# Kernel optimization log

Hardware: AMD Instinct MI355X
Metric: run time of the kernel (lower is better)

## Reference

```python
import jax
import jax.numpy as jnp
import numpy as np

N = 16384        # total input points (single batch: o = [N])
C_IN = 64        # in_planes
C_OUT = 128      # out_planes
NSAMPLE = 16     # neighbors per sampled point
STRIDE = 4       # -> new_stride = 2, FPS samples N//2 points
BN_EPS = 1e-5


def setup_inputs() -> dict:
    key = jax.random.key(0)
    k1, k2, k3 = jax.random.split(key, 3)
    p = jax.random.normal(k1, (N, 3), dtype=jnp.float32)
    x = jax.random.normal(k2, (N, C_IN), dtype=jnp.float32)
    o = jnp.array([N], dtype=jnp.int32)  # single-batch offset
    W = jax.random.normal(k3, (3 + C_IN, C_OUT), dtype=jnp.float32) * 0.05
    gamma = jnp.ones((C_OUT,), dtype=jnp.float32)
    beta = jnp.zeros((C_OUT,), dtype=jnp.float32)
    return {"p": p, "x": x, "o": o, "W": W, "gamma": gamma, "beta": beta}


def fps(p, m):
    """Furthest point sampling: returns m indices into p [N,3], starting at 0."""
    n = p.shape[0]
    def step(carry, _):
        dists, last = carry  # dists: [N] min sq-dist to selected set
        d = jnp.sum((p - p[last]) ** 2, axis=-1)
        dists = jnp.minimum(dists, d)
        nxt = jnp.argmax(dists).astype(jnp.int32)
        return (dists, nxt), nxt
    init = (jnp.full((n,), 1e10, dtype=p.dtype), jnp.int32(0))
    _, rest = jax.lax.scan(step, init, None, length=m - 1)
    return jnp.concatenate([jnp.zeros((1,), jnp.int32), rest])


def knn_idx(q, p, k):
    """Indices of k nearest points in p [N,3] for each query in q [m,3]."""
    d = (jnp.sum(q * q, -1, keepdims=True)
         - 2.0 * (q @ p.T)
         + jnp.sum(p * p, -1))  # [m, N]
    _, idx = jax.lax.top_k(-d, k)
    return idx


def group_mlp_pool(q, p, x, W, gamma, beta):
    """queryandgroup(use_xyz=True) -> linear -> BN(train) -> ReLU -> maxpool(nsample)."""
    idx = knn_idx(q, p, NSAMPLE)                      # [m, k]
    rel = p[idx] - q[:, None, :]                       # [m, k, 3] relative xyz
    feats = jnp.concatenate([rel, x[idx]], axis=-1)    # [m, k, 3+C_IN]
    h = feats @ W                                      # [m, k, C_OUT]
    # BatchNorm1d in training mode: stats over (m, k) per channel
    mean = jnp.mean(h, axis=(0, 1))
    var = jnp.var(h, axis=(0, 1))
    h = (h - mean) * jax.lax.rsqrt(var + BN_EPS) * gamma + beta
    h = jax.nn.relu(h)
    return jnp.max(h, axis=1)                          # [m, C_OUT]


def reference(p, x, o, W, gamma, beta):
    m_total = N // (STRIDE // 2)       # 8192 sampled points
    idx = fps(p, m_total)
    m1 = m_total // 2 + m_total % 2    # first half (ceil)
    idx1, idx2 = idx[:m1], idx[m1:]
    n_p, n_p2 = p[idx1], p[idx2]
    x1 = group_mlp_pool(n_p, p, x, W, gamma, beta)
    x2 = group_mlp_pool(n_p2, p, x, W, gamma, beta)
    n_o = jnp.array([m1], dtype=jnp.int32)
    n_o2 = jnp.array([m_total - m1], dtype=jnp.int32)
    return (n_p, x1, n_o, n_p2, x2, n_o2)
```

## Files before the change

kernel.cpp:

```cpp
#include <hip/hip_runtime.h>

#define N_PTS 16384
#define M_TOTAL 8192
#define M1 4096

#define OUT_NP   0
#define OUT_X1   12288
#define OUT_NO   536576
#define OUT_NP2  536577
#define OUT_X2   548865
#define OUT_NO2  1073153

#define POOL_C 64

__global__ void k0_init(const float* __restrict__ p, float* __restrict__ sump,
                        float* __restrict__ px, float* __restrict__ py, float* __restrict__ pz,
                        float* __restrict__ out, int* __restrict__ flag, int* __restrict__ fidx,
                        double* __restrict__ bn) {
    int i = blockIdx.x * 256 + threadIdx.x;
    if (i == 0) { out[OUT_NO] = 4096.0f; out[OUT_NO2] = 4096.0f; atomicExch(flag, 0); }
    if (i < 512) bn[i] = 0.0;
    if (i < M_TOTAL) fidx[i] = (i == 0) ? 0 : -1;
    if (i < N_PTS) {
        float x = p[3*i], y = p[3*i+1], z = p[3*i+2];
        px[i] = x; py[i] = y; pz[i] = z;
        sump[i] = __fadd_rn(__fadd_rn(__fmul_rn(x,x), __fmul_rn(y,y)), __fmul_rn(z,z));
    }
}

__device__ __forceinline__ unsigned spread4(unsigned v) {
    return (v & 1u) | ((v & 2u) << 2) | ((v & 4u) << 4) | ((v & 8u) << 6);
}
__device__ __forceinline__ float bb_d2(float qx, float qy, float qz,
                                       float mnx, float mxx, float mny, float mxy,
                                       float mnz, float mxz) {
    float ax = fmaxf(fmaxf(__fsub_rn(mnx, qx), __fsub_rn(qx, mxx)), 0.0f);
    float ay = fmaxf(fmaxf(__fsub_rn(mny, qy), __fsub_rn(qy, mxy)), 0.0f);
    float az = fmaxf(fmaxf(__fsub_rn(mnz, qz), __fsub_rn(qz, mxz)), 0.0f);
    return __fadd_rn(__fadd_rn(__fmul_rn(ax,ax), __fmul_rn(ay,ay)), __fmul_rn(az,az));
}
__device__ __forceinline__ float pt_d2(float ax, float ay, float az,
                                       float bx, float by, float bz) {
    float dx = __fsub_rn(ax,bx), dy = __fsub_rn(ay,by), dz = __fsub_rn(az,bz);
    return __fadd_rn(__fadd_rn(__fmul_rn(dx,dx), __fmul_rn(dy,dy)), __fmul_rn(dz,dz));
}
__device__ __forceinline__ float wave_max64(float v) {
    v = fmaxf(v, __int_as_float(__builtin_amdgcn_update_dpp(0, __float_as_int(v), 0x111, 0xf, 0xf, true)));
    v = fmaxf(v, __int_as_float(__builtin_amdgcn_update_dpp(0, __float_as_int(v), 0x112, 0xf, 0xf, true)));
    v = fmaxf(v, __int_as_float(__builtin_amdgcn_update_dpp(0, __float_as_int(v), 0x114, 0xf, 0xf, true)));
    v = fmaxf(v, __int_as_float(__builtin_amdgcn_update_dpp(0, __float_as_int(v), 0x118, 0xf, 0xf, true)));
    v = fmaxf(v, __int_as_float(__builtin_amdgcn_update_dpp(0, __float_as_int(v), 0x142, 0xf, 0xf, true)));
    v = fmaxf(v, __int_as_float(__builtin_amdgcn_update_dpp(0, __float_as_int(v), 0x143, 0xf, 0xf, true)));
    return __int_as_float(__builtin_amdgcn_readlane(__float_as_int(v), 63));
}

__global__ __launch_bounds__(1024) void k1_fps(
    const float* __restrict__ p,
    float* __restrict__ rx, float* __restrict__ ry, float* __restrict__ rz,
    int* __restrict__ rid,
    int* __restrict__ fidx, float* __restrict__ out, int* __restrict__ flag,
    const float* __restrict__ px, const float* __restrict__ py,
    const float* __restrict__ pz, const float* __restrict__ sump,
    const float* __restrict__ xin, const float* __restrict__ W,
    float* __restrict__ hmax, float* __restrict__ hmin,
    double* __restrict__ bn)
{
    int tid = threadIdx.x, lane = tid & 63, wv = tid >> 6;

    __shared__ int hist[4096];
    __shared__ float sred[16][6];
    __shared__ int wsum[16];
    __shared__ float4 pool4[POOL_C];
    __shared__ unsigned ppk[POOL_C];
    __shared__ float4 barr4[POOL_C+1];
    __shared__ unsigned skeys[POOL_C];
    __shared__ float fdv[16];
    __shared__ unsigned fdk[16];
    __shared__ unsigned mcell;
    __shared__ float s_invm;
    __shared__ int s_cutbin;
    __shared__ unsigned s_cutbits;
    __shared__ unsigned s_fkey;
    __shared__ int bcnt, tcell;
    __shared__ float sdk[4][16][64];
    __shared__ int   sik[4][16][64];

    if (blockIdx.x != 0) {
        float a0 = 1.0f + tid, a1 = 2.0f, a2 = 3.0f, a3 = 4.0f;
        const float hb = 1.0000001f, hc = 1e-9f;
        if (wv < 4) {
            int g = (blockIdx.x - 1) * 4 + wv;
            for (int jq = 0; jq < 9; ++jq) {
                int q = g + 1020 * jq;
                if (q >= M_TOTAL) break;
                int qi = -1;
                for (;;) {
                    if (lane == 0)
                        qi = __hip_atomic_load(&fidx[q], __ATOMIC_RELAXED, __HIP_MEMORY_SCOPE_AGENT);
                    qi = __shfl(qi, 0);
                    if (qi >= 0) break;
#pragma unroll
                    for (int u = 0; u < 256; ++u) {
                        a0 = __fmaf_rn(a0, hb, hc); a1 = __fmaf_rn(a1, hb, hc);
                        a2 = __fmaf_rn(a2, hb, hc); a3 = __fmaf_rn(a3, hb, hc);
                    }
                }
                float qx = px[qi], qy = py[qi], qz = pz[qi], sq = sump[qi];
                float bd[16]; int bi[16];
#pragma unroll
                for (int k = 0; k < 16; ++k) { bd[k] = 3.4e38f; bi[k] = 0x7fffffff; }
                for (int j0 = 0; j0 < N_PTS; j0 += 64) {
                    int j = j0 + lane;
                    float dot = __fmaf_rn(pz[j], qz, __fmaf_rn(py[j], qy, __fmul_rn(px[j], qx)));
                    float d = __fadd_rn(__fsub_rn(sq, __fmul_rn(2.0f, dot)), sump[j]);
                    if (d < bd[15]) {
                        float cdv = d; int ci = j;
#pragma unroll
                        for (int k = 0; k < 16; ++k) {
                            if (cdv < bd[k]) { float td = bd[k]; int ti = bi[k]; bd[k] = cdv; bi[k] = ci; cdv = td; ci = ti; }
                        }
                    }
                }
#pragma unroll
                for (int k = 0; k < 16; ++k) { sdk[wv][k][lane] = bd[k]; sik[wv][k][lane] = bi[k]; }
                int njr[16];
                int pos = 0;
#pragma unroll
                for (int r = 0; r < 16; ++r) {
                    float hd = (pos < 16) ? sdk[wv][pos][lane] : 3.4e38f;
                    int   hi2 = (pos < 16) ? sik[wv][pos][lane] : 0x7fffffff;
                    float md = hd; int mi = hi2;
#pragma unroll
                    for (int off = 1; off < 64; off <<= 1) {
                        float od = __shfl_xor(md, off);
                        int   oi = __shfl_xor(mi, off);
                        if (od < md || (od == md && oi < mi)) { md = od; mi = oi; }
                    }
                    if (hi2 == mi && pos < 16) pos++;
                    njr[r] = mi;
                }

                float hmx0 = -3.4e38f, hmn0 = 3.4e38f, hmx1 = -3.4e38f, hmn1 = 3.4e38f;
                double sm0 = 0.0, sq0 = 0.0, sm1 = 0.0, sq1 = 0.0;
#pragma unroll
                for (int s2 = 0; s2 < 16; ++s2) {
                    int nj = njr[s2];
                    float acc0 = 0.0f, acc1 = 0.0f;
                    {
                        float f0 = p[3*nj+0] - qx;
                        acc0 = __fmaf_rn(f0, W[0*128 + lane], acc0);
                        acc1 = __fmaf_rn(f0, W[0*128 + 64 + lane], acc1);
                        float f1 = p[3*nj+1] - qy;
                        acc0 = __fmaf_rn(f1, W[1*128 + lane], acc0);
                        acc1 = __fmaf_rn(f1, W[1*128 + 64 + lane], acc1);
                        float f2 = p[3*nj+2] - qz;
                        acc0 = __fmaf_rn(f2, W[2*128 + lane], acc0);
                        acc1 = __fmaf_rn(f2, W[2*128 + 64 + lane], acc1);
                    }
                    const float* xr = &xin[nj*64];
                    for (int j = 3; j < 67; ++j) {
                        float f = xr[j-3];
                        acc0 = __fmaf_rn(f, W[j*128 + lane], acc0);
                        acc1 = __fmaf_rn(f, W[j*128 + 64 + lane], acc1);
                    }
                    hmx0 = fmaxf(hmx0, acc0); hmn0 = fminf(hmn0, acc0);
                    hmx1 = fmaxf(hmx1, acc1); hmn1 = fminf(hmn1, acc1);
                    sm0 += (double)acc0; sq0 += (double)acc0 * (double)acc0;
                    sm1 += (double)acc1; sq1 += (double)acc1 * (double)acc1;
                }
                hmax[q*128 + lane]      = hmx0;  hmax[q*128 + 64 + lane] = hmx1;
                hmin[q*128 + lane]      = hmn0;  hmin[q*128 + 64 + lane] = hmn1;
                int hb2 = (q >= M1) ? 128 : 0;
                atomicAdd(&bn[hb2 + lane],            sm0);
                atomicAdd(&bn[hb2 + 64 + lane],       sm1);
                atomicAdd(&bn[256 + hb2 + lane],      sq0);
                atomicAdd(&bn[256 + hb2 + 64 + lane], sq1);
            }
        }
        for (;;) {
#pragma unroll
            for (int u = 0; u < 512; ++u) {
                a0 = __fmaf_rn(a0, hb, hc); a1 = __fmaf_rn(a1, hb, hc);
                a2 = __fmaf_rn(a2, hb, hc); a3 = __fmaf_rn(a3, hb, hc);
            }
            int done = 0;
            if (lane == 0)
                done = __hip_atomic_load(flag, __ATOMIC_RELAXED, __HIP_MEMORY_SCOPE_AGENT);
            done = __shfl(done, 0);
            if (done) break;
        }
        __asm__ volatile("" :: "v"(a0), "v"(a1), "v"(a2), "v"(a3));
        return;
    }

    float mnx = 3.4e38f, mny = 3.4e38f, mnz = 3.4e38f;
    float mxx = -3.4e38f, mxy = -3.4e38f, mxz = -3.4e38f;
#pragma unroll
    for (int k = 0; k < 16; ++k) {
        int i = tid + 1024*k;
        float x = p[3*i], y = p[3*i+1], z = p[3*i+2];
        mnx = fminf(mnx, x); mxx = fmaxf(mxx, x);
        mny = fminf(mny, y); mxy = fmaxf(mxy, y);
        mnz = fminf(mnz, z); mxz = fmaxf(mxz, z);
    }
#pragma unroll
    for (int off = 1; off < 64; off <<= 1) {
        mnx = fminf(mnx, __shfl_xor(mnx, off)); mxx = fmaxf(mxx, __shfl_xor(mxx, off));
        mny = fminf(mny, __shfl_xor(mny, off)); mxy = fmaxf(mxy, __shfl_xor(mxy, off));
        mnz = fminf(mnz, __shfl_xor(mnz, off)); mxz = fmaxf(mxz, __shfl_xor(mxz, off));
    }
    if (lane == 0) {
        sred[wv][0] = mnx; sred[wv][1] = mxx; sred[wv][2] = mny;
        sred[wv][3] = mxy; sred[wv][4] = mnz; sred[wv][5] = mxz;
    }
    for (int j = tid; j < 4096; j += 1024) hist[j] = 0;
    __syncthreads();
    mnx = sred[0][0]; mxx = sred[0][1]; mny = sred[0][2];
    mxy = sred[0][3]; mnz = sred[0][4]; mxz = sred[0][5];
    for (int w2 = 1; w2 < 16; ++w2) {
        mnx = fminf(mnx, sred[w2][0]); mxx = fmaxf(mxx, sred[w2][1]);
        mny = fminf(mny, sred[w2][2]); mxy = fmaxf(mxy, sred[w2][3]);
        mnz = fminf(mnz, sred[w2][4]); mxz = fmaxf(mxz, sred[w2][5]);
    }
    float sx = 16.0f / fmaxf(mxx - mnx, 1e-20f);
    float sy = 16.0f / fmaxf(mxy - mny, 1e-20f);
    float sz = 16.0f / fmaxf(mxz - mnz, 1e-20f);

    int mcode[16];
#pragma unroll
    for (int k = 0; k < 16; ++k) {
        int i = tid + 1024*k;
        float x = p[3*i], y = p[3*i+1], z = p[3*i+2];
        int cx = min(15, (int)((x - mnx) * sx));
        int cy = min(15, (int)((y - mny) * sy));
        int cz = min(15, (int)((z - mnz) * sz));
        int m = (int)(spread4((unsigned)cx) | (spread4((unsigned)cy) << 1) | (spread4((unsigned)cz) << 2));
        mcode[k] = m;
        atomicAdd(&hist[m], 1);
    }
    __syncthreads();
    {
        int c0 = hist[4*tid], c1 = hist[4*tid+1], c2 = hist[4*tid+2], c3 = hist[4*tid+3];
        int lsum = c0 + c1 + c2 + c3;
        int incl = lsum;
#pragma unroll
        for (int off = 1; off < 64; off <<= 1) {
            int n = __shfl_up(incl, off);
            if (lane >= off) incl += n;
        }
        if (lane == 63) wsum[wv] = incl;
        __syncthreads();
        int woff = 0;
        for (int j = 0; j < wv; ++j) woff += wsum[j];
        int excl = woff + incl - lsum;
        hist[4*tid]   = excl;
        hist[4*tid+1] = excl + c0;
        hist[4*tid+2] = excl + c0 + c1;
        hist[4*tid+3] = excl + c0 + c1 + c2;
    }
    __syncthreads();
#pragma unroll
    for (int k = 0; k < 16; ++k) {
        int i = tid + 1024*k;
        int pos = atomicAdd(&hist[mcode[k]], 1);
        rx[pos] = p[3*i]; ry[pos] = p[3*i+1]; rz[pos] = p[3*i+2];
        rid[pos] = i;
    }
    __syncthreads();

    int base = tid * 16;
    float ld[16];
    float bmnx = 3.4e38f, bmny = 3.4e38f, bmnz = 3.4e38f;
    float bmxx = -3.4e38f, bmxy = -3.4e38f, bmxz = -3.4e38f;
#pragma unroll
    for (int k = 0; k < 16; ++k) {
        float x = rx[base+k], y = ry[base+k], z = rz[base+k];
        ld[k] = 1e10f;
        bmnx = fminf(bmnx, x); bmxx = fmaxf(bmxx, x);
        bmny = fminf(bmny, y); bmxy = fmaxf(bmxy, y);
        bmnz = fminf(bmnz, z); bmxz = fmaxf(bmxz, z);
    }
    float wsmnx = bmnx, wsmxx = bmxx, wsmny = bmny, wsmxy = bmxy, wsmnz = bmnz, wsmxz = bmxz;
#pragma unroll
    for (int off = 1; off < 64; off <<= 1) {
        wsmnx = fminf(wsmnx, __shfl_xor(wsmnx, off)); wsmxx = fmaxf(wsmxx, __shfl_xor(wsmxx, off));
        wsmny = fminf(wsmny, __shfl_xor(wsmny, off)); wsmxy = fmaxf(wsmxy, __shfl_xor(wsmxy, off));
        wsmnz = fminf(wsmnz, __shfl_xor(wsmnz, off)); wsmxz = fmaxf(wsmxz, __shfl_xor(wsmxz, off));
    }
    float gmax = 1e10f, wave_gmax = 1e10f;

    if (tid == 0) {
        float x0 = p[0], y0 = p[1], z0 = p[2];
        out[OUT_NP+0] = x0; out[OUT_NP+1] = y0; out[OUT_NP+2] = z0;
        barr4[0] = make_float4(x0, y0, z0, 0.0f);
        skeys[0] = 0u;
        bcnt = 1; tcell = 1; mcell = 0u;
    }

    for (;;) {
        __syncthreads();
        int t_now = tcell;
        int s = bcnt;
        if (tid < s)
            __hip_atomic_store(&fidx[t_now - s + tid], (int)skeys[tid], __ATOMIC_RELAXED, __HIP_MEMORY_SCOPE_AGENT);
        if (t_now >= M_TOTAL) break;

        {
            bool dirtyw = false;
            if (lane < s) {
                float4 cc = barr4[lane];
                dirtyw = bb_d2(cc.x, cc.y, cc.z, wsmnx, wsmxx, wsmny, wsmxy, wsmnz, wsmxz) < wave_gmax;
            }
            unsigned long long mm = __ballot(dirtyw);
            if (mm) {
                float gx[16], gy[16], gz[16];
#pragma unroll
                for (int k = 0; k < 16; ++k) { gx[k] = rx[base+k]; gy[k] = ry[base+k]; gz[k] = rz[base+k]; }
                while (mm) {
                    int b = __builtin_ctzll(mm); mm &= mm - 1;
                    float4 cc = barr4[b];
                    if (bb_d2(cc.x, cc.y, cc.z, bmnx, bmxx, bmny, bmxy, bmnz, bmxz) < gmax) {
#pragma unroll
                        for (int k = 0; k < 16; ++k)
                            ld[k] = fminf(ld[k], pt_d2(gx[k], gy[k], gz[k], cc.x, cc.y, cc.z));
                    }
                }
            }
        }
        gmax = ld[0];
#pragma unroll
        for (int k = 1; k < 16; ++k) gmax = fmaxf(gmax, ld[k]);
        wave_gmax = wave_max64(gmax);
        if (lane == 0) atomicMax(&mcell, __float_as_uint(wave_gmax));
        if (tid < 130) hist[tid] = 0;
        __syncthreads();
        if (tid == 0) { s_invm = 1.0f / __uint_as_float(mcell); mcell = 0u; }
        __syncthreads();
        float invm = s_invm;
#pragma unroll
        for (int k = 0; k < 16; ++k) {
            unsigned u = __float_as_uint(__fmul_rn(ld[k], invm));
            if (u >= 0x3F000000u) {
                int bin = 16256 - (int)(u >> 16);
                bin = bin < 0 ? 0 : (bin > 128 ? 128 : bin);
                atomicAdd(&hist[bin], 1);
            }
        }
        __syncthreads();
        if (wv == 0) {
            int b0 = hist[2*lane], b1 = hist[2*lane+1];
            int pair = b0 + b1;
            int incl = pair;
#pragma unroll
            for (int off = 1; off < 64; off <<= 1) { int n = __shfl_up(incl, off); if (lane >= off) incl += n; }
            int before = incl - pair;
            int cb = 0;
            if (before + b0 <= POOL_C) cb = 2*lane + 1;
            if (before + pair <= POOL_C) cb = 2*lane + 2;
            if (lane == 63) { if (incl + hist[128] <= POOL_C) cb = 129; }
#pragma unroll
            for (int off = 1; off < 64; off <<= 1) cb = max(cb, __shfl_xor(cb, off));
            if (lane == 0) { s_cutbin = cb; s_cutbits = (unsigned)(16257 - cb) << 16; }
        }
        __syncthreads();

        unsigned cutbits = s_cutbits;
        int cl = 0;
#pragma unroll
        for (int k = 0; k < 16; ++k)
            cl += (__float_as_uint(__fmul_rn(ld[k], invm)) >= cutbits) ? 1 : 0;
        int inc3 = cl;
#pragma unroll
        for (int off = 1; off < 64; off <<= 1) { int n = __shfl_up(inc3, off); if (lane >= off) inc3 += n; }
        if (lane == 63) wsum[wv] = inc3;
        __syncthreads();
        int woff2 = 0, ptot = 0;
        for (int j = 0; j < 16; ++j) { int wsj = wsum[j]; if (j < wv) woff2 += wsj; ptot += wsj; }

        if (s_cutbin == 0 || ptot == 0) {
            float bv = -1.0f; unsigned bk = 0xffffffffu;
#pragma unroll
            for (int k = 0; k < 16; ++k) {
                unsigned kk = ((unsigned)rid[base+k] << 14) | (unsigned)(base + k);
                bool better = (ld[k] > bv) || (ld[k] == bv && kk < bk);
                bv = better ? ld[k] : bv; bk = better ? kk : bk;
            }
#pragma unroll
            for (int off = 1; off < 64; off <<= 1) {
                float ov = __shfl_xor(bv, off); unsigned ok = __shfl_xor(bk, off);
                bool better = (ov > bv) || (ov == bv && ok < bk);
                bv = better ? ov : bv; bk = better ? ok : bk;
            }
            if (lane == 0) { fdv[wv] = bv; fdk[wv] = bk; }
            __syncthreads();
            if (tid < 64) {
                float v2 = (tid < 16) ? fdv[tid] : -1.0f;
                unsigned k2v = (tid < 16) ? fdk[tid] : 0xffffffffu;
#pragma unroll
                for (int off = 1; off < 16; off <<= 1) {
                    float ov = __shfl_xor(v2, off); unsigned ok = __shfl_xor(k2v, off);
                    bool better = (ov > v2) || (ov == v2 && ok < k2v);
                    v2 = better ? ov : v2; k2v = better ? ok : k2v;
                }
                if (tid == 0) {
                    s_fkey = k2v;
                    int pos = (int)(k2v & 16383u);
                    __hip_atomic_store(&fidx[t_now], (int)(k2v >> 14), __ATOMIC_RELAXED, __HIP_MEMORY_SCOPE_AGENT);
                    float wx = rx[pos], wy = ry[pos], wz = rz[pos];
                    int o = (t_now < M1) ? (OUT_NP + 3*t_now) : (OUT_NP2 + 3*(t_now - M1));
                    out[o] = wx; out[o+1] = wy; out[o+2] = wz;
                    tcell = t_now + 1; bcnt = 0;
                }
            }
            __syncthreads();
            {
                int pos = (int)(s_fkey & 16383u);
                float wx = rx[pos], wy = ry[pos], wz = rz[pos];
                if (bb_d2(wx, wy, wz, bmnx, bmxx, bmny, bmxy, bmnz, bmxz) < gmax) {
#pragma unroll
                    for (int k = 0; k < 16; ++k)
                        ld[k] = fminf(ld[k], pt_d2(rx[base+k], ry[base+k], rz[base+k], wx, wy, wz));
                }
            }
            continue;
        }

        int nb = woff2 + inc3 - cl;
#pragma unroll
        for (int k = 0; k < 16; ++k) {
            if (__float_as_uint(__fmul_rn(ld[k], invm)) >= cutbits) {
                pool4[nb] = make_float4(rx[base+k], ry[base+k], rz[base+k], ld[k]);
                ppk[nb] = (unsigned)rid[base+k];
                nb++;
            }
        }
        if (tid >= ptot && tid < POOL_C) {
            pool4[tid] = make_float4(0.0f, 0.0f, 0.0f, 0.0f);
            ppk[tid] = 0x7fffffffu;
        }
        __syncthreads();

        if (wv == 0) {
            __builtin_amdgcn_s_setprio(3);
            float4 e = pool4[lane];
            float ex = e.x, ey = e.y, ez = e.z, dv = e.w;
            unsigned key = ppk[lane];
            int tl = t_now, bc = 0;
            float mw = wave_max64(dv);
            while (__float_as_uint(__fmul_rn(mw, invm)) >= cutbits) {
                unsigned long long tie = __ballot(dv == mw);
                int wl;
                if (__popcll(tie) == 1) {
                    wl = (int)__builtin_ctzll(tie);
                } else {
                    unsigned kk = (dv == mw) ? key : 0xffffffffu;
#pragma unroll
                    for (int off = 1; off < 64; off <<= 1) kk = min(kk, (unsigned)__shfl_xor((int)kk, off));
                    tie = __ballot(dv == mw && key == kk);
                    wl = (int)__builtin_ctzll(tie);
                }
                float wx = __int_as_float(__builtin_amdgcn_readlane(__float_as_int(ex), wl));
                float wy = __int_as_float(__builtin_amdgcn_readlane(__float_as_int(ey), wl));
                float wz = __int_as_float(__builtin_amdgcn_readlane(__float_as_int(ez), wl));
                unsigned wk = (unsigned)__builtin_amdgcn_readlane((int)key, wl);
                if (lane == 0) {
                    skeys[bc] = wk;
                    int o = (tl < M1) ? (OUT_NP + 3*tl) : (OUT_NP2 + 3*(tl - M1));
                    out[o] = wx; out[o+1] = wy; out[o+2] = wz;
                    barr4[bc] = make_float4(wx, wy, wz, 0.0f);
                }
                ++bc; ++tl;
                if (tl >= M_TOTAL) break;
                dv = fminf(dv, pt_d2(ex, ey, ez, wx, wy, wz));
                mw = wave_max64(dv);
            }
            __builtin_amdgcn_s_setprio(0);
            if (lane == 0) { bcnt = bc; tcell = tl; }
        }
    }

    if (tid == 0) atomicExch(flag, 1);
}

__global__ void k35_stats(const double* __restrict__ bn,
                          const float* __restrict__ gamma, const float* __restrict__ beta,
                          float* __restrict__ scale, float* __restrict__ shift) {
    int t = threadIdx.x;
    int c = t & 127;
    double mean = bn[t] / 65536.0;
    double var  = bn[256 + t] / 65536.0 - mean*mean;
    double sc   = (double)gamma[c] / sqrt(var + 1e-5);
    scale[t] = (float)sc;
    shift[t] = (float)((double)beta[c] - mean*sc);
}

__global__ __launch_bounds__(256) void k4_out(const float* __restrict__ hmax, const float* __restrict__ hmin,
                                              const float* __restrict__ scale, const float* __restrict__ shift,
                                              float* __restrict__ out) {
    int e = blockIdx.x * 256 + threadIdx.x;
    int q = e >> 7, c = e & 127;
    int half = (q >= M1) ? 1 : 0;
    float a = scale[half*128 + c], b = shift[half*128 + c];
    float v = (a >= 0.0f) ? hmax[e] : hmin[e];
    float r = fmaxf(0.0f, a*v + b);
    int off = half ? (OUT_X2 + (q - M1)*128 + c) : (OUT_X1 + q*128 + c);
    out[off] = r;
}

extern "C" void kernel_launch(void* const* d_in, const int* in_sizes, int n_in,
                              void* d_out, int out_size, void* d_ws, size_t ws_size,
                              hipStream_t stream) {
    const float* p     = (const float*)d_in[0];
    const float* x     = (const float*)d_in[1];
    const float* W     = (const float*)d_in[3];
    const float* gamma = (const float*)d_in[4];
    const float* beta  = (const float*)d_in[5];
    float* out = (float*)d_out;

    float* wsf  = (float*)d_ws;
    float* sump = wsf;
    float* px   = wsf + 16384;
    float* py   = wsf + 32768;
    float* pz   = wsf + 49152;
    int*   fidx = (int*)(wsf + 65536);
    float* hmax = wsf + 204800;
    float* hmin = wsf + 1253376;
    float* rxp  = (float*)((char*)d_ws + 9207808);
    float* ryp  = rxp + 16384;
    float* rzp  = ryp + 16384;
    int*   ridp = (int*)(rzp + 16384);
    int*   flag = (int*)(ridp + 16384);
    double* bn  = (double*)((char*)d_ws + 9207808 + 4*65536 + 256);
    float* scale = (float*)(bn + 512);
    float* shift = scale + 256;

    k0_init <<<64,   256, 0, stream>>>(p, sump, px, py, pz, out, flag, fidx, bn);
    k1_fps  <<<256, 1024, 0, stream>>>(p, rxp, ryp, rzp, ridp, fidx, out, flag,
                                       px, py, pz, sump, x, W, hmax, hmin, bn);
    k35_stats<<<1,   256, 0, stream>>>(bn, gamma, beta, scale, shift);
    k4_out  <<<4096, 256, 0, stream>>>(hmax, hmin, scale, shift, out);
}
```

Before: 5.282 ms.

## Overlap FPS distance updates with wave-0 batch selection via shared progress flag

Wave 0 now publishes a workgroup-scope progress counter in shared memory as it selects FPS points from the candidate pool. The other waves no longer wait for the whole batch. They poll the counter and apply min-distance updates for each newly published point while wave 0 keeps selecting. At the start of the next iteration only wave 0 applies the previous batch. This is meant to hide the serial selection loop behind the other waves' distance updates. The cost is spin-polling with s_sleep, extra atomics, and more subtle ordering between the waves.

```diff
diff --git a/kernel.cpp b/kernel.cpp
--- a/kernel.cpp
+++ b/kernel.cpp
@@ -82,6 +82,7 @@
     __shared__ unsigned s_cutbits;
     __shared__ unsigned s_fkey;
     __shared__ int bcnt, tcell;
+    __shared__ int sprog;
     __shared__ float sdk[4][16][64];
     __shared__ int   sik[4][16][64];
 
@@ -305,7 +306,7 @@
             __hip_atomic_store(&fidx[t_now - s + tid], (int)skeys[tid], __ATOMIC_RELAXED, __HIP_MEMORY_SCOPE_AGENT);
         if (t_now >= M_TOTAL) break;
 
-        {
+        if (wv == 0) {
             bool dirtyw = false;
             if (lane < s) {
                 float4 cc = barr4[lane];
@@ -438,6 +439,7 @@
             pool4[tid] = make_float4(0.0f, 0.0f, 0.0f, 0.0f);
             ppk[tid] = 0x7fffffffu;
         }
+        if (tid == 0) sprog = 0;
         __syncthreads();
 
         if (wv == 0) {
@@ -468,6 +470,8 @@
                     int o = (tl < M1) ? (OUT_NP + 3*tl) : (OUT_NP2 + 3*(tl - M1));
                     out[o] = wx; out[o+1] = wy; out[o+2] = wz;
                     barr4[bc] = make_float4(wx, wy, wz, 0.0f);
+                    if ((bc & 3) == 3)
+                        __hip_atomic_store(&sprog, bc + 1, __ATOMIC_RELEASE, __HIP_MEMORY_SCOPE_WORKGROUP);
                 }
                 ++bc; ++tl;
                 if (tl >= M_TOTAL) break;
@@ -475,7 +479,39 @@
                 mw = wave_max64(dv);
             }
             __builtin_amdgcn_s_setprio(0);
-            if (lane == 0) { bcnt = bc; tcell = tl; }
+            if (lane == 0) {
+                bcnt = bc; tcell = tl;
+                __hip_atomic_store(&sprog, bc | 0x10000, __ATOMIC_RELEASE, __HIP_MEMORY_SCOPE_WORKGROUP);
+            }
+        } else {
+            int applied = 0;
+            bool ldd2 = false;
+            float gx[16], gy[16], gz[16];
+            for (;;) {
+                int snap = __hip_atomic_load(&sprog, __ATOMIC_ACQUIRE, __HIP_MEMORY_SCOPE_WORKGROUP);
+                int avail = snap & 0xFFFF;
+                bool fin = (snap & 0x10000) != 0;
+                if (avail > applied) {
+                    for (; applied < avail; ++applied) {
+                        float4 cc = barr4[applied];
+                        if (bb_d2(cc.x, cc.y, cc.z, wsmnx, wsmxx, wsmny, wsmxy, wsmnz, wsmxz) < wave_gmax) {
+                            if (!ldd2) {
+#pragma unroll
+                                for (int k = 0; k < 16; ++k) { gx[k] = rx[base+k]; gy[k] = ry[base+k]; gz[k] = rz[base+k]; }
+                                ldd2 = true;
+                            }
+                            if (bb_d2(cc.x, cc.y, cc.z, bmnx, bmxx, bmny, bmxy, bmnz, bmxz) < gmax) {
+#pragma unroll
+                                for (int k = 0; k < 16; ++k)
+                                    ld[k] = fminf(ld[k], pt_d2(gx[k], gy[k], gz[k], cc.x, cc.y, cc.z));
+                            }
+                        }
+                    }
+                } else if (!fin) {
+                    __builtin_amdgcn_s_sleep(2);
+                }
+                if (fin) break;
+            }
         }
     }
 
```

After: 6.403 ms. +21.2%, slower.
